# Optimization experiments

Hardware: AMD Instinct MI355X
Metric: run time of the kernel (lower is better)

Reference implementation:

```python
import jax, jax.numpy as jnp
import numpy as np


def _log_kernel(ks, sigma):
    ax = np.arange(-(ks // 2), ks // 2 + 1, dtype=np.float64)
    xx, yy = np.meshgrid(ax, ax, indexing='ij')
    r2 = xx ** 2 + yy ** 2
    gaussian = np.exp(-r2 / (2 * sigma ** 2))
    laplacian = -1.0 / (np.pi * sigma ** 4) * (1.0 - r2 / (2 * sigma ** 2))
    k = laplacian * gaussian
    k = k / np.sum(np.abs(k))
    return jnp.asarray(k, jnp.float32)


def _hpf_kernel(ks):
    if ks == 3:
        k = np.array([[-1, -1, -1], [-1, 8, -1], [-1, -1, -1]], dtype=np.float32)
    else:  # 5
        k = -np.ones((5, 5), dtype=np.float32)
        k[2, 2] = 24.0
    return jnp.asarray(k)


def _lpf_kernel():
    k = np.array([[1, 2, 1], [2, 4, 2], [1, 2, 1]], dtype=np.float32) / 16.0
    return jnp.asarray(k)


def _gabor_kernel(angle, frequency=0.1, sigma_x=2.0, sigma_y=2.0):
    theta = np.radians(angle)
    x, y = np.meshgrid(np.linspace(-3, 3, 7), np.linspace(-3, 3, 7))
    x_t = x * np.cos(theta) + y * np.sin(theta)
    y_t = -x * np.sin(theta) + y * np.cos(theta)
    g = np.exp(-(x_t ** 2 / sigma_x ** 2 + y_t ** 2 / sigma_y ** 2) / 2.0) * np.cos(2 * np.pi * frequency * x_t)
    g = g / np.sum(np.abs(g))
    return jnp.asarray(g, jnp.float32)


def _dwconv(x, k2d, pad):
    # depthwise conv: same single-channel kernel applied to every channel
    C = x.shape[1]
    kern = jnp.broadcast_to(k2d[None, None], (C, 1) + k2d.shape)  # (C,1,kh,kw)
    return jax.lax.conv_general_dilated(
        x, kern, window_strides=(1, 1), padding=[(pad, pad), (pad, pad)],
        feature_group_count=C, dimension_numbers=('NCHW', 'OIHW', 'NCHW'))


def _squash(z):
    # (tanh(z*0.1)+1)/2
    return (jnp.tanh(z * 0.1) + 1.0) * 0.5


def setup_inputs() -> dict:
    key = jax.random.key(0)
    x = jax.random.normal(key, (16, 3, 512, 512), dtype=jnp.float32)
    return {"x": x, "use_gabor": 1}


def reference(x, use_gabor):
    # 'original'
    original = x
    # 'lpf'
    lpf = _dwconv(x, _lpf_kernel(), pad=1)
    # 'log': multi-scale LoG -> squash -> elementwise max over scales
    log3 = _dwconv(x, _log_kernel(3, 0.8), pad=1)
    log5 = _dwconv(x, _log_kernel(5, 1.0), pad=2)
    log7 = _dwconv(x, _log_kernel(7, 1.4), pad=3)
    log_out = jnp.maximum(jnp.maximum(_squash(log3), _squash(log5)), _squash(log7))
    # 'hpf'
    hpf3 = _dwconv(x, _hpf_kernel(3), pad=1)
    hpf5 = _dwconv(x, _hpf_kernel(5), pad=2)
    hpf_out = jnp.maximum(_squash(hpf3), _squash(hpf5))
    outs = (original, lpf, log_out, hpf_out)
    if use_gabor:
        gab = None
        for angle in (0, 45, 90, 135):
            r = jnp.tanh(_dwconv(x, _gabor_kernel(angle), pad=3) * 0.1)
            gab = r if gab is None else jnp.maximum(gab, r)
        outs = outs + (gab,)
    return outs
```

## Files before the change

### kernel.cpp

```cpp
#include <hip/hip_runtime.h>

#define IMG_H 512
#define IMG_W 512
#define TILE_W 64
#define TILE_H 16
#define LDSW 72
#define LDSH 22
#define NTHREADS 256


constexpr double PI_D = 3.141592653589793238462643383279502884;

constexpr double cexp(double x) {
  double term = 1.0, sum = 1.0;
  for (int n = 1; n < 48; ++n) { term *= x / n; sum += term; }
  return sum;
}
constexpr double ccos(double x) {
  double term = 1.0, sum = 1.0;
  for (int n = 1; n < 24; ++n) {
    term *= -x * x / ((2.0 * n - 1.0) * (2.0 * n));
    sum += term;
  }
  return sum;
}
constexpr double csin(double x) {
  double term = x, sum = x;
  for (int n = 1; n < 24; ++n) {
    term *= -x * x / ((2.0 * n) * (2.0 * n + 1.0));
    sum += term;
  }
  return sum;
}
constexpr double cabs_(double x) { return x < 0 ? -x : x; }

struct KTabs {
  float lpf[9];
  float log3[9];
  float log5[25];
  float log7[49];
  float hpf3[9];
  float hpf5[25];
  float gab[4][49];
};

constexpr void fill_log(int ks, double sigma, float* out) {
  double buf[49] = {};
  double s = 0.0;
  const int h = ks / 2;
  for (int i = 0; i < ks; ++i) {
    for (int j = 0; j < ks; ++j) {
      const double xi = (double)(i - h);
      const double yj = (double)(j - h);
      const double r2 = xi * xi + yj * yj;
      const double g = cexp(-r2 / (2.0 * sigma * sigma));
      const double lap = -1.0 / (PI_D * sigma * sigma * sigma * sigma) *
                         (1.0 - r2 / (2.0 * sigma * sigma));
      buf[i * ks + j] = lap * g;
      s += cabs_(lap * g);
    }
  }
  for (int k = 0; k < ks * ks; ++k) out[k] = (float)(buf[k] / s);
}

constexpr void fill_gabor(double ang_deg, float* out) {
  const double th = ang_deg * PI_D / 180.0;
  const double ct = ccos(th), st = csin(th);
  double buf[49] = {};
  double s = 0.0;
  for (int i = 0; i < 7; ++i) {
    for (int j = 0; j < 7; ++j) {
      const double xv = (double)(j - 3);
      const double yv = (double)(i - 3);
      const double xt = xv * ct + yv * st;
      const double yt = -xv * st + yv * ct;
      const double g = cexp(-(xt * xt / 4.0 + yt * yt / 4.0) / 2.0) *
                       ccos(2.0 * PI_D * 0.1 * xt);
      buf[i * 7 + j] = g;
      s += cabs_(g);
    }
  }
  for (int k = 0; k < 49; ++k) out[k] = (float)(buf[k] / s);
}

constexpr KTabs make_tabs() {
  KTabs t{};
  const double lv[9] = {1, 2, 1, 2, 4, 2, 1, 2, 1};
  for (int k = 0; k < 9; ++k) t.lpf[k] = (float)(lv[k] / 16.0);
  for (int k = 0; k < 9; ++k) t.hpf3[k] = -1.0f;
  t.hpf3[4] = 8.0f;
  for (int k = 0; k < 25; ++k) t.hpf5[k] = -1.0f;
  t.hpf5[12] = 24.0f;
  fill_log(3, 0.8, t.log3);
  fill_log(5, 1.0, t.log5);
  fill_log(7, 1.4, t.log7);
  fill_gabor(0.0, t.gab[0]);
  fill_gabor(45.0, t.gab[1]);
  fill_gabor(90.0, t.gab[2]);
  fill_gabor(135.0, t.gab[3]);
  return t;
}

constexpr KTabs KT = make_tabs();


__device__ __forceinline__ float fast_tanh(float x) {
  float e = __builtin_amdgcn_exp2f(x * 2.8853900817779268f);
  return 1.0f - 2.0f * __builtin_amdgcn_rcpf(e + 1.0f);
}
__device__ __forceinline__ float squash_from(float z) {
  return fmaf(fast_tanh(0.1f * z), 0.5f, 0.5f);
}

__global__ __launch_bounds__(NTHREADS)
void msif_kernel(const float* __restrict__ x, float* __restrict__ out,
                 int planes, int do_gab) {
  __shared__ float tile[LDSH * LDSW];
  const int tid = threadIdx.x;
  const int tx = tid & 15;
  const int ty = tid >> 4;
  const int x0 = blockIdx.x * TILE_W;
  const int y0 = blockIdx.y * TILE_H;
  const int plane = blockIdx.z;
  const float* __restrict__ in = x + (size_t)plane * (IMG_H * IMG_W);

  const int gx0 = x0 - 4;
  const int gy0 = y0 - 3;
  for (int k = tid; k < LDSH * (LDSW / 4); k += NTHREADS) {
    int r = k / (LDSW / 4);
    int cc = (k - r * (LDSW / 4)) * 4;
    int gy = gy0 + r;
    int gx = gx0 + cc;
    float4 v = make_float4(0.f, 0.f, 0.f, 0.f);
    if ((unsigned)gy < IMG_H) {
      const float* rowp = in + (size_t)gy * IMG_W;
      if (gx >= 0 && gx + 3 < IMG_W) {
        v = *(const float4*)(rowp + gx);
      } else {
        float t0 = 0.f, t1 = 0.f, t2 = 0.f, t3 = 0.f;
        if ((unsigned)(gx + 0) < IMG_W) t0 = rowp[gx + 0];
        if ((unsigned)(gx + 1) < IMG_W) t1 = rowp[gx + 1];
        if ((unsigned)(gx + 2) < IMG_W) t2 = rowp[gx + 2];
        if ((unsigned)(gx + 3) < IMG_W) t3 = rowp[gx + 3];
        v = make_float4(t0, t1, t2, t3);
      }
    }
    *(float4*)&tile[r * LDSW + cc] = v;
  }
  __syncthreads();

  float l7[4] = {}, l5[4] = {}, l3[4] = {};
  float h5[4] = {}, h3[4] = {}, lp[4] = {};
  float g0[4] = {}, g1[4] = {}, g2[4] = {}, g3[4] = {};

#pragma unroll
  for (int ir = 0; ir < 7; ++ir) {
    const float4* p = (const float4*)&tile[(ty + ir) * LDSW + 4 * tx];
    float4 w0 = p[0], w1 = p[1], w2 = p[2];
    float w[12] = {w0.x, w0.y, w0.z, w0.w, w1.x, w1.y, w1.z, w1.w,
                   w2.x, w2.y, w2.z, w2.w};

#pragma unroll
    for (int dx = 0; dx < 7; ++dx) {
      const float c7 = KT.log7[ir * 7 + dx];
      const float cg0 = KT.gab[0][ir * 7 + dx];
      const float cg1 = KT.gab[1][ir * 7 + dx];
      const float cg2 = KT.gab[2][ir * 7 + dx];
      const float cg3 = KT.gab[3][ir * 7 + dx];
#pragma unroll
      for (int c = 0; c < 4; ++c) {
        const float v = w[c + dx + 1];
        l7[c] = fmaf(v, c7, l7[c]);
        g0[c] = fmaf(v, cg0, g0[c]);
        g1[c] = fmaf(v, cg1, g1[c]);
        g2[c] = fmaf(v, cg2, g2[c]);
        g3[c] = fmaf(v, cg3, g3[c]);
      }
    }
    if (ir >= 1 && ir <= 5) {
      const int kr = ir - 1;
#pragma unroll
      for (int dx = 0; dx < 5; ++dx) {
        const float c5 = KT.log5[kr * 5 + dx];
        const float ch5 = KT.hpf5[kr * 5 + dx];
#pragma unroll
        for (int c = 0; c < 4; ++c) {
          const float v = w[c + dx + 2];
          l5[c] = fmaf(v, c5, l5[c]);
          h5[c] = fmaf(v, ch5, h5[c]);
        }
      }
    }
    if (ir >= 2 && ir <= 4) {
      const int kr = ir - 2;
#pragma unroll
      for (int dx = 0; dx < 3; ++dx) {
        const float cl = KT.lpf[kr * 3 + dx];
        const float c3 = KT.log3[kr * 3 + dx];
        const float ch3 = KT.hpf3[kr * 3 + dx];
#pragma unroll
        for (int c = 0; c < 4; ++c) {
          const float v = w[c + dx + 3];
          lp[c] = fmaf(v, cl, lp[c]);
          l3[c] = fmaf(v, c3, l3[c]);
          h3[c] = fmaf(v, ch3, h3[c]);
        }
      }
    }
  }

  const int X = x0 + 4 * tx;
  const int yo = y0 + ty;
  const size_t fs = (size_t)planes * (IMG_H * IMG_W);
  const size_t off = (size_t)plane * (IMG_H * IMG_W) + (size_t)yo * IMG_W + X;

  float4 orig = *(const float4*)&tile[(ty + 3) * LDSW + 4 * tx + 4];
  *(float4*)(out + off) = orig;

  float lo[4], ho[4], go[4];
#pragma unroll
  for (int c = 0; c < 4; ++c) {
    lo[c] = squash_from(fmaxf(fmaxf(l3[c], l5[c]), l7[c]));
    ho[c] = squash_from(fmaxf(h3[c], h5[c]));
    go[c] = fast_tanh(0.1f * fmaxf(fmaxf(g0[c], g1[c]), fmaxf(g2[c], g3[c])));
  }
  *(float4*)(out + fs + off) = make_float4(lp[0], lp[1], lp[2], lp[3]);
  *(float4*)(out + 2 * fs + off) = make_float4(lo[0], lo[1], lo[2], lo[3]);
  *(float4*)(out + 3 * fs + off) = make_float4(ho[0], ho[1], ho[2], ho[3]);
  if (do_gab)
    *(float4*)(out + 4 * fs + off) = make_float4(go[0], go[1], go[2], go[3]);
}

extern "C" void kernel_launch(void* const* d_in, const int* in_sizes, int n_in,
                              void* d_out, int out_size, void* d_ws, size_t ws_size,
                              hipStream_t stream) {
  const float* x = (const float*)d_in[0];
  float* out = (float*)d_out;
  const int plane_elems = IMG_H * IMG_W;
  const int planes = in_sizes[0] / plane_elems;
  const int do_gab = (out_size >= 5 * in_sizes[0]) ? 1 : 0;

  dim3 grid(IMG_W / TILE_W, IMG_H / TILE_H, planes);
  msif_kernel<<<grid, NTHREADS, 0, stream>>>(x, out, planes, do_gab);
}
```

Before: 317.3 us.

## Split fused filter kernel into three lighter kernels for higher occupancy

```diff
diff --git a/kernel.cpp b/kernel.cpp
--- a/kernel.cpp
+++ b/kernel.cpp
@@ -112,18 +112,9 @@
   return fmaf(fast_tanh(0.1f * z), 0.5f, 0.5f);
 }
 
-__global__ __launch_bounds__(NTHREADS)
-void msif_kernel(const float* __restrict__ x, float* __restrict__ out,
-                 int planes, int do_gab) {
-  __shared__ float tile[LDSH * LDSW];
-  const int tid = threadIdx.x;
-  const int tx = tid & 15;
-  const int ty = tid >> 4;
-  const int x0 = blockIdx.x * TILE_W;
-  const int y0 = blockIdx.y * TILE_H;
-  const int plane = blockIdx.z;
-  const float* __restrict__ in = x + (size_t)plane * (IMG_H * IMG_W);
-
+__device__ __forceinline__ void stage_tile(const float* __restrict__ in,
+                                           float* __restrict__ tile, int x0,
+                                           int y0, int tid) {
   const int gx0 = x0 - 4;
   const int gy0 = y0 - 3;
   for (int k = tid; k < LDSH * (LDSW / 4); k += NTHREADS) {
@@ -137,32 +128,164 @@
       if (gx >= 0 && gx + 3 < IMG_W) {
         v = *(const float4*)(rowp + gx);
       } else {
-        float t0 = 0.f, t1 = 0.f, t2 = 0.f, t3 = 0.f;
-        if ((unsigned)(gx + 0) < IMG_W) t0 = rowp[gx + 0];
-        if ((unsigned)(gx + 1) < IMG_W) t1 = rowp[gx + 1];
-        if ((unsigned)(gx + 2) < IMG_W) t2 = rowp[gx + 2];
-        if ((unsigned)(gx + 3) < IMG_W) t3 = rowp[gx + 3];
-        v = make_float4(t0, t1, t2, t3);
+        if ((unsigned)(gx + 0) < IMG_W) v.x = rowp[gx + 0];
+        if ((unsigned)(gx + 1) < IMG_W) v.y = rowp[gx + 1];
+        if ((unsigned)(gx + 2) < IMG_W) v.z = rowp[gx + 2];
+        if ((unsigned)(gx + 3) < IMG_W) v.w = rowp[gx + 3];
       }
     }
     *(float4*)&tile[r * LDSW + cc] = v;
   }
+}
+
+#define LOADW12(ROW)                                                        \
+  {                                                                         \
+    const float4* p = (const float4*)&tile[(ROW)*LDSW + 4 * tx];            \
+    float4 w0 = p[0], w1 = p[1], w2 = p[2];                                 \
+    w[0] = w0.x; w[1] = w0.y; w[2] = w0.z; w[3] = w0.w;                     \
+    w[4] = w1.x; w[5] = w1.y; w[6] = w1.z; w[7] = w1.w;                     \
+    w[8] = w2.x; w[9] = w2.y; w[10] = w2.z; w[11] = w2.w;                   \
+  }
+
+
+__global__ __launch_bounds__(NTHREADS, 6)
+void k_log(const float* __restrict__ x, float* __restrict__ out, int planes) {
+  __shared__ float tile[LDSH * LDSW];
+  const int tid = threadIdx.x;
+  const int tx = tid & 15;
+  const int ty = tid >> 4;
+  const int x0 = blockIdx.x * TILE_W;
+  const int y0 = blockIdx.y * TILE_H;
+  const int plane = blockIdx.z;
+  const float* __restrict__ in = x + (size_t)plane * (IMG_H * IMG_W);
+
+  stage_tile(in, tile, x0, y0, tid);
   __syncthreads();
 
-  float l7[4] = {}, l5[4] = {}, l3[4] = {};
-  float h5[4] = {}, h3[4] = {}, lp[4] = {};
-  float g0[4] = {}, g1[4] = {}, g2[4] = {}, g3[4] = {};
+  float l7[4] = {}, l5[4] = {}, l3[4] = {}, lp[4] = {};
+  float w[12];
 
 #pragma unroll
   for (int ir = 0; ir < 7; ++ir) {
-    const float4* p = (const float4*)&tile[(ty + ir) * LDSW + 4 * tx];
-    float4 w0 = p[0], w1 = p[1], w2 = p[2];
-    float w[12] = {w0.x, w0.y, w0.z, w0.w, w1.x, w1.y, w1.z, w1.w,
-                   w2.x, w2.y, w2.z, w2.w};
-
+    LOADW12(ty + ir);
 #pragma unroll
     for (int dx = 0; dx < 7; ++dx) {
       const float c7 = KT.log7[ir * 7 + dx];
+#pragma unroll
+      for (int c = 0; c < 4; ++c) l7[c] = fmaf(w[c + dx + 1], c7, l7[c]);
+    }
+    if (ir >= 1 && ir <= 5) {
+      const int kr = ir - 1;
+#pragma unroll
+      for (int dx = 0; dx < 5; ++dx) {
+        const float c5 = KT.log5[kr * 5 + dx];
+#pragma unroll
+        for (int c = 0; c < 4; ++c) l5[c] = fmaf(w[c + dx + 2], c5, l5[c]);
+      }
+    }
+    if (ir >= 2 && ir <= 4) {
+      const int kr = ir - 2;
+#pragma unroll
+      for (int dx = 0; dx < 3; ++dx) {
+        const float cl = KT.lpf[kr * 3 + dx];
+        const float c3 = KT.log3[kr * 3 + dx];
+#pragma unroll
+        for (int c = 0; c < 4; ++c) {
+          const float v = w[c + dx + 3];
+          lp[c] = fmaf(v, cl, lp[c]);
+          l3[c] = fmaf(v, c3, l3[c]);
+        }
+      }
+    }
+  }
+
+  const size_t fs = (size_t)planes * (IMG_H * IMG_W);
+  const size_t off = (size_t)plane * (IMG_H * IMG_W) +
+                     (size_t)(y0 + ty) * IMG_W + (x0 + 4 * tx);
+
+  const float4 orig = *(const float4*)&tile[(ty + 3) * LDSW + 4 * tx + 4];
+  *(float4*)(out + off) = orig;
+
+  float lo[4];
+#pragma unroll
+  for (int c = 0; c < 4; ++c)
+    lo[c] = squash_from(fmaxf(fmaxf(l3[c], l5[c]), l7[c]));
+  *(float4*)(out + fs + off) = make_float4(lp[0], lp[1], lp[2], lp[3]);
+  *(float4*)(out + 2 * fs + off) = make_float4(lo[0], lo[1], lo[2], lo[3]);
+}
+
+
+__global__ __launch_bounds__(NTHREADS, 8)
+void k_hpf(const float* __restrict__ x, float* __restrict__ out, int planes) {
+  __shared__ float tile[LDSH * LDSW];
+  const int tid = threadIdx.x;
+  const int tx = tid & 15;
+  const int ty = tid >> 4;
+  const int x0 = blockIdx.x * TILE_W;
+  const int y0 = blockIdx.y * TILE_H;
+  const int plane = blockIdx.z;
+  const float* __restrict__ in = x + (size_t)plane * (IMG_H * IMG_W);
+
+  stage_tile(in, tile, x0, y0, tid);
+  __syncthreads();
+
+  float h5[4] = {}, h3[4] = {};
+  float w[12];
+
+#pragma unroll
+  for (int ir = 1; ir <= 5; ++ir) {
+    LOADW12(ty + ir);
+    const int kr = ir - 1;
+#pragma unroll
+    for (int dx = 0; dx < 5; ++dx) {
+      const float ch5 = KT.hpf5[kr * 5 + dx];
+#pragma unroll
+      for (int c = 0; c < 4; ++c) h5[c] = fmaf(w[c + dx + 2], ch5, h5[c]);
+    }
+    if (ir >= 2 && ir <= 4) {
+      const int k3 = ir - 2;
+#pragma unroll
+      for (int dx = 0; dx < 3; ++dx) {
+        const float ch3 = KT.hpf3[k3 * 3 + dx];
+#pragma unroll
+        for (int c = 0; c < 4; ++c) h3[c] = fmaf(w[c + dx + 3], ch3, h3[c]);
+      }
+    }
+  }
+
+  const size_t fs = (size_t)planes * (IMG_H * IMG_W);
+  const size_t off = (size_t)plane * (IMG_H * IMG_W) +
+                     (size_t)(y0 + ty) * IMG_W + (x0 + 4 * tx);
+
+  float ho[4];
+#pragma unroll
+  for (int c = 0; c < 4; ++c) ho[c] = squash_from(fmaxf(h3[c], h5[c]));
+  *(float4*)(out + 3 * fs + off) = make_float4(ho[0], ho[1], ho[2], ho[3]);
+}
+
+
+__global__ __launch_bounds__(NTHREADS, 6)
+void k_gab(const float* __restrict__ x, float* __restrict__ out, int planes) {
+  __shared__ float tile[LDSH * LDSW];
+  const int tid = threadIdx.x;
+  const int tx = tid & 15;
+  const int ty = tid >> 4;
+  const int x0 = blockIdx.x * TILE_W;
+  const int y0 = blockIdx.y * TILE_H;
+  const int plane = blockIdx.z;
+  const float* __restrict__ in = x + (size_t)plane * (IMG_H * IMG_W);
+
+  stage_tile(in, tile, x0, y0, tid);
+  __syncthreads();
+
+  float g0[4] = {}, g1[4] = {}, g2[4] = {}, g3[4] = {};
+  float w[12];
+
+#pragma unroll
+  for (int ir = 0; ir < 7; ++ir) {
+    LOADW12(ty + ir);
+#pragma unroll
+    for (int dx = 0; dx < 7; ++dx) {
       const float cg0 = KT.gab[0][ir * 7 + dx];
       const float cg1 = KT.gab[1][ir * 7 + dx];
       const float cg2 = KT.gab[2][ir * 7 + dx];
@@ -170,65 +293,23 @@
 #pragma unroll
       for (int c = 0; c < 4; ++c) {
         const float v = w[c + dx + 1];
-        l7[c] = fmaf(v, c7, l7[c]);
         g0[c] = fmaf(v, cg0, g0[c]);
         g1[c] = fmaf(v, cg1, g1[c]);
         g2[c] = fmaf(v, cg2, g2[c]);
         g3[c] = fmaf(v, cg3, g3[c]);
       }
     }
-    if (ir >= 1 && ir <= 5) {
-      const int kr = ir - 1;
-#pragma unroll
-      for (int dx = 0; dx < 5; ++dx) {
-        const float c5 = KT.log5[kr * 5 + dx];
-        const float ch5 = KT.hpf5[kr * 5 + dx];
-#pragma unroll
-        for (int c = 0; c < 4; ++c) {
-          const float v = w[c + dx + 2];
-          l5[c] = fmaf(v, c5, l5[c]);
-          h5[c] = fmaf(v, ch5, h5[c]);
-        }
-      }
-    }
-    if (ir >= 2 && ir <= 4) {
-      const int kr = ir - 2;
-#pragma unroll
-      for (int dx = 0; dx < 3; ++dx) {
-        const float cl = KT.lpf[kr * 3 + dx];
-        const float c3 = KT.log3[kr * 3 + dx];
-        const float ch3 = KT.hpf3[kr * 3 + dx];
-#pragma unroll
-        for (int c = 0; c < 4; ++c) {
-          const float v = w[c + dx + 3];
-          lp[c] = fmaf(v, cl, lp[c]);
-          l3[c] = fmaf(v, c3, l3[c]);
-          h3[c] = fmaf(v, ch3, h3[c]);
-        }
-      }
-    }
-  }
-
-  const int X = x0 + 4 * tx;
-  const int yo = y0 + ty;
+  }
+
   const size_t fs = (size_t)planes * (IMG_H * IMG_W);
-  const size_t off = (size_t)plane * (IMG_H * IMG_W) + (size_t)yo * IMG_W + X;
-
-  float4 orig = *(const float4*)&tile[(ty + 3) * LDSW + 4 * tx + 4];
-  *(float4*)(out + off) = orig;
-
-  float lo[4], ho[4], go[4];
-#pragma unroll
-  for (int c = 0; c < 4; ++c) {
-    lo[c] = squash_from(fmaxf(fmaxf(l3[c], l5[c]), l7[c]));
-    ho[c] = squash_from(fmaxf(h3[c], h5[c]));
+  const size_t off = (size_t)plane * (IMG_H * IMG_W) +
+                     (size_t)(y0 + ty) * IMG_W + (x0 + 4 * tx);
+
+  float go[4];
+#pragma unroll
+  for (int c = 0; c < 4; ++c)
     go[c] = fast_tanh(0.1f * fmaxf(fmaxf(g0[c], g1[c]), fmaxf(g2[c], g3[c])));
-  }
-  *(float4*)(out + fs + off) = make_float4(lp[0], lp[1], lp[2], lp[3]);
-  *(float4*)(out + 2 * fs + off) = make_float4(lo[0], lo[1], lo[2], lo[3]);
-  *(float4*)(out + 3 * fs + off) = make_float4(ho[0], ho[1], ho[2], ho[3]);
-  if (do_gab)
-    *(float4*)(out + 4 * fs + off) = make_float4(go[0], go[1], go[2], go[3]);
+  *(float4*)(out + 4 * fs + off) = make_float4(go[0], go[1], go[2], go[3]);
 }
 
 extern "C" void kernel_launch(void* const* d_in, const int* in_sizes, int n_in,
@@ -241,5 +322,7 @@
   const int do_gab = (out_size >= 5 * in_sizes[0]) ? 1 : 0;
 
   dim3 grid(IMG_W / TILE_W, IMG_H / TILE_H, planes);
-  msif_kernel<<<grid, NTHREADS, 0, stream>>>(x, out, planes, do_gab);
-}
+  k_log<<<grid, NTHREADS, 0, stream>>>(x, out, planes);
+  k_hpf<<<grid, NTHREADS, 0, stream>>>(x, out, planes);
+  if (do_gab) k_gab<<<grid, NTHREADS, 0, stream>>>(x, out, planes);
+}
```

After: 353.6 us. 1.11x slower.
